# Optimization experiments

Measured on AMD Instinct MI355X. Metric: run time of the kernel, lower is better.

The kernel has to match this reference:

```python
import jax, jax.numpy as jnp
import numpy as np

# hardcoded constants from Model.sample_regions / gather_regions / __init__
RADIUS = 0.4
REGIONS = 50
BALL_K = 1000
TOP_K = 4
NEIGHBORHOOD = 128
COURSE = 512


def square_distance(src, dst):
    """src [B,N,C], dst [B,M,C] -> squared dists [B,N,M]."""
    d = -2.0 * jnp.einsum('bnc,bmc->bnm', src, dst)
    d = d + jnp.sum(src * src, -1)[:, :, None]
    d = d + jnp.sum(dst * dst, -1)[:, None, :]
    return d


def furthest_point_sample(xyz, npoint):
    """xyz [B,N,3] -> indices [B,npoint] (deterministic start at point 0)."""
    B, N, _ = xyz.shape
    barange = jnp.arange(B)

    def body(carry, _):
        dist, last = carry                      # dist [B,N], last [B] int32
        centroid = xyz[barange, last]           # [B,3]
        d = jnp.sum((xyz - centroid[:, None, :]) ** 2, -1)
        dist = jnp.minimum(dist, d)
        nxt = jnp.argmax(dist, axis=-1).astype(jnp.int32)
        return (dist, nxt), last

    init = (jnp.full((B, N), 1e10, xyz.dtype), jnp.zeros((B,), jnp.int32))
    _, idxs = jax.lax.scan(body, init, None, length=npoint)
    return jnp.transpose(idxs)                  # [B, npoint]


def knn_point(k, xyz, new_xyz):
    """k-NN of new_xyz [B,S,3] among xyz [B,N,3] -> idx [B,S,k]."""
    d = square_distance(new_xyz, xyz)
    _, idx = jax.lax.top_k(-d, k)
    return idx


def gather_xyz(xyz, idx):
    """xyz [B,N,3], idx [B,S] -> [B,S,3]."""
    B = xyz.shape[0]
    return xyz[jnp.arange(B)[:, None], idx]


def gather_regions(p_xyz, a_xyz, radius):
    """p_xyz [B,N,3] points, a_xyz [B,A,3] anchors -> [B, TOP_K*NEIGHBORHOOD, 3]."""
    B = p_xyz.shape[0]
    d2 = square_distance(a_xyz, p_xyz)                       # [B,A,N]
    counts = jnp.minimum(jnp.sum(d2 < radius * radius, axis=2), BALL_K)
    _, topk_idx = jax.lax.top_k(counts, TOP_K)               # densest anchors [B,TOP_K]
    sel = gather_xyz(a_xyz, topk_idx)                        # [B,TOP_K,3]
    nidx = knn_point(NEIGHBORHOOD, p_xyz, sel)               # [B,TOP_K,NB]
    neigh = p_xyz[jnp.arange(B)[:, None, None], nidx]        # [B,TOP_K,NB,3]
    return neigh.reshape(B, TOP_K * NEIGHBORHOOD, 3)


def sample_regions(p_xyz, regions, r):
    anchors_idx = furthest_point_sample(p_xyz, regions)
    anchors = gather_xyz(p_xyz, anchors_idx)
    return gather_regions(p_xyz, anchors, r)


def setup_inputs() -> dict:
    key = jax.random.key(0)
    points = jax.random.normal(key, (16, 3, 16384), dtype=jnp.float32)
    return {"points": points}


def reference(points):
    # points [B,3,N] -> p_xyz [B,N,3]
    p_xyz = jnp.transpose(points, (0, 2, 1))
    roi1 = sample_regions(p_xyz, REGIONS, RADIUS)            # [B,512,3]
    roi2 = sample_regions(p_xyz, REGIONS, RADIUS)            # [B,512,3] (a == b == 0.4)
    fps_idx = furthest_point_sample(p_xyz, COURSE)           # [B,512]
    fps_pts = gather_xyz(p_xyz, fps_idx)                     # [B,512,3]
    return jnp.concatenate([roi1, roi2, fps_pts], axis=1)    # [B,1536,3]
```

## Files before the change

kernel.cpp:

```cpp
#include <hip/hip_runtime.h>
#include <stdint.h>

#define NPTS 16384
#define BATCH 16
#define FPS_N 512
#define NANCH 50
#define TOPK 4
#define NBH 128
#define BALLK 1000

#define FT 512
#define PAIRS 16

#define OFF_X2 0
#define OFF_Y2 65536
#define OFF_FPSIDX 131072
#define OFF_CNT    (OFF_FPSIDX + 2048)
#define OFF_WRED   (OFF_CNT + 256)
#define OFF_T4     (OFF_WRED + 128)
#define OFF_KNN    (OFF_T4 + 16)
#define SMEM_TOTAL (OFF_KNN + 512)

#define CTRL_XOR1 0xB1
#define CTRL_XOR2 0x4E
#define CTRL_ROR4 0x124
#define CTRL_ROR8 0x128

#define DPP_MAX64(v, CTRL) do {                                                   \
  unsigned int _lo = (unsigned int)(v);                                           \
  unsigned int _hi = (unsigned int)((v) >> 32);                                   \
  unsigned int _slo = (unsigned int)__builtin_amdgcn_update_dpp((int)_lo, (int)_lo, CTRL, 0xf, 0xf, false); \
  unsigned int _shi = (unsigned int)__builtin_amdgcn_update_dpp((int)_hi, (int)_hi, CTRL, 0xf, 0xf, false); \
  unsigned long long _o = (((unsigned long long)_shi) << 32) | _slo;              \
  if (_o > (v)) (v) = _o;                                                         \
} while (0)

#define DPP_MIN64(v, CTRL) do {                                                   \
  unsigned int _lo = (unsigned int)(v);                                           \
  unsigned int _hi = (unsigned int)((v) >> 32);                                   \
  unsigned int _slo = (unsigned int)__builtin_amdgcn_update_dpp((int)_lo, (int)_lo, CTRL, 0xf, 0xf, false); \
  unsigned int _shi = (unsigned int)__builtin_amdgcn_update_dpp((int)_hi, (int)_hi, CTRL, 0xf, 0xf, false); \
  unsigned long long _o = (((unsigned long long)_shi) << 32) | _slo;              \
  if (_o < (v)) (v) = _o;                                                         \
} while (0)

#define SWZ16_MIN64(v) do {                                                       \
  unsigned int _lo = (unsigned int)(v), _hi = (unsigned int)((v) >> 32);          \
  unsigned int _slo = (unsigned int)__builtin_amdgcn_ds_swizzle((int)_lo, 0x401f);\
  unsigned int _shi = (unsigned int)__builtin_amdgcn_ds_swizzle((int)_hi, 0x401f);\
  unsigned long long _o = (((unsigned long long)_shi) << 32) | _slo;              \
  if (_o < (v)) (v) = _o;                                                         \
} while (0)

#define SHF32_MIN64(v) do {                                                       \
  unsigned long long _o = __shfl_xor((v), 32, 64);                                \
  if (_o < (v)) (v) = _o;                                                         \
} while (0)

__device__ __forceinline__ uint32_t f2key(float f) {
  uint32_t u = __float_as_uint(f);
  return (u & 0x80000000u) ? ~u : (u | 0x80000000u);
}

__global__ __launch_bounds__(FT, 2) void mega_kernel(const float* __restrict__ pts,
                                                     float* __restrict__ out) {
  extern __shared__ char smem[];
  float2* __restrict__ X2 = (float2*)(smem + OFF_X2);
  float2* __restrict__ Y2 = (float2*)(smem + OFF_Y2);
  int* __restrict__ fpsidx = (int*)(smem + OFF_FPSIDX);
  int* __restrict__ cnt = (int*)(smem + OFF_CNT);
  unsigned long long* __restrict__ wred = (unsigned long long*)(smem + OFF_WRED);
  int* __restrict__ t4 = (int*)(smem + OFF_T4);
  int* __restrict__ knnidx = (int*)(smem + OFF_KNN);

  const int bid = blockIdx.x;
  const bool isFps = bid < BATCH;
  const int b = isFps ? bid : ((bid - BATCH) >> 2);
  const int j = isFps ? 0 : ((bid - BATCH) & 3);
  const int nsteps = isFps ? FPS_N : NANCH;

  const int t = threadIdx.x;
  const int wS = __builtin_amdgcn_readfirstlane(t >> 6);
  const float* __restrict__ px = pts + (size_t)b * 3 * NPTS;
  const float* __restrict__ py = px + NPTS;
  const float* __restrict__ pz = py + NPTS;

  float2 z2[PAIRS], dist2[PAIRS];
#pragma unroll
  for (int k = 0; k < PAIRS; ++k) {
    const int i2 = (k << 10) + (t << 1);
    X2[(k << 9) + t] = *(const float2*)&px[i2];
    Y2[(k << 9) + t] = *(const float2*)&py[i2];
    z2[k] = *(const float2*)&pz[i2];
    dist2[k] = make_float2(1e10f, 1e10f);
  }
  if (t == 0) fpsidx[0] = 0;
  float bx = px[0], by = py[0], bz = pz[0];
  __syncthreads();

  for (int step = 1; step < nsteps; ++step) {
    const float nbx = -bx, nby = -by, nbz = -bz;
    const float2 nbx2 = make_float2(nbx, nbx);
    const float2 nby2 = make_float2(nby, nby);
    const float2 nbz2 = make_float2(nbz, nbz);
    float run = -1.0f;
#pragma unroll
    for (int k = 0; k < PAIRS; ++k) {
      const float2 Xp = X2[(k << 9) + t];
      const float2 Yp = Y2[(k << 9) + t];
      float2 t0, t1, t2;
      asm("v_pk_add_f32 %0, %3, %6\n\t"
          "v_pk_add_f32 %1, %4, %7\n\t"
          "v_pk_add_f32 %2, %5, %8\n\t"
          "v_pk_mul_f32 %0, %0, %0\n\t"
          "v_pk_mul_f32 %1, %1, %1\n\t"
          "v_pk_mul_f32 %2, %2, %2\n\t"
          "v_pk_add_f32 %0, %0, %1\n\t"
          "v_pk_add_f32 %0, %0, %2"
          : "=&v"(t0), "=&v"(t1), "=&v"(t2)
          : "v"(Xp), "v"(Yp), "v"(z2[k]), "v"(nbx2), "v"(nby2), "v"(nbz2));
      dist2[k].x = fminf(dist2[k].x, t0.x);
      dist2[k].y = fminf(dist2[k].y, t0.y);
      asm("v_max3_f32 %0, %0, %1, %2"
          : "+v"(run) : "v"(dist2[k].x), "v"(dist2[k].y));
    }
    uint32_t m = __float_as_uint(run);
    {
      uint32_t s;
      s = (uint32_t)__builtin_amdgcn_update_dpp((int)m, (int)m, CTRL_XOR1, 0xf, 0xf, false); m = m > s ? m : s;
      s = (uint32_t)__builtin_amdgcn_update_dpp((int)m, (int)m, CTRL_XOR2, 0xf, 0xf, false); m = m > s ? m : s;
      s = (uint32_t)__builtin_amdgcn_update_dpp((int)m, (int)m, CTRL_ROR4, 0xf, 0xf, false); m = m > s ? m : s;
      s = (uint32_t)__builtin_amdgcn_update_dpp((int)m, (int)m, CTRL_ROR8, 0xf, 0xf, false); m = m > s ? m : s;
      s = (uint32_t)__builtin_amdgcn_ds_swizzle((int)m, 0x401f);                              m = m > s ? m : s;
      s = (uint32_t)__shfl_xor((int)m, 32, 64);                                              m = m > s ? m : s;
    }
    const float gmaxf = __uint_as_float(m);
    uint32_t widx_w = 0xFFFFFFFFu;
#pragma unroll
    for (int k = 0; k < PAIRS; ++k) {
      const unsigned long long b0 = __ballot(dist2[k].x == gmaxf);
      const unsigned long long b1 = __ballot(dist2[k].y == gmaxf);
      const unsigned long long cb = b0 | b1;
      if (cb) {
        const int l = (int)__builtin_ctzll(cb);
        const uint32_t p = ((b0 >> l) & 1ull) ? 0u : 1u;
        const uint32_t cand = ((uint32_t)k << 10) + ((uint32_t)((wS << 6) | l) << 1) + p;
        widx_w = widx_w < cand ? widx_w : cand;
      }
    }
    const unsigned long long key =
        ((unsigned long long)m << 32) | (uint32_t)(~widx_w);
    const int par = step & 1;
    if ((t & 63) == 0) wred[par * 8 + wS] = key;
    __syncthreads();
    unsigned long long g = wred[par * 8 + (t & 7)];
    DPP_MAX64(g, CTRL_XOR1);
    DPP_MAX64(g, CTRL_XOR2);
    DPP_MAX64(g, CTRL_ROR4);
    const uint32_t widx = ~(uint32_t)g;
    if (t == 0) fpsidx[step] = (int)widx;
    const int si = __builtin_amdgcn_readfirstlane((int)widx);
    bx = px[si]; by = py[si]; bz = pz[si];
  }

  if (isFps) {
    __syncthreads();
    const int idx = fpsidx[t];
    const float X = px[idx], Y = py[idx], Z = pz[idx];
    float* o = out + ((size_t)b * 1536 + 1024 + t) * 3;
    o[0] = X; o[1] = Y; o[2] = Z;
    return;
  }

  const float R2 = (float)(0.4 * 0.4);

  if (t < 64) cnt[t] = 0;
  __syncthreads();
  for (int a = 0; a < NANCH; ++a) {
    const int ai = fpsidx[a];
    const float ax = px[ai], ay = py[ai], az = pz[ai];
    const float asum = __fadd_rn(__fadd_rn(__fmul_rn(ax, ax), __fmul_rn(ay, ay)),
                                 __fmul_rn(az, az));
    int local = 0;
#pragma unroll
    for (int k = 0; k < PAIRS; ++k) {
      const float2 Xp = X2[(k << 9) + t];
      const float2 Yp = Y2[(k << 9) + t];
      const float2 Zp = z2[k];
      {
        const float dot = __fadd_rn(__fadd_rn(__fmul_rn(ax, Xp.x), __fmul_rn(ay, Yp.x)),
                                    __fmul_rn(az, Zp.x));
        const float ps = __fadd_rn(__fadd_rn(__fmul_rn(Xp.x, Xp.x), __fmul_rn(Yp.x, Yp.x)),
                                   __fmul_rn(Zp.x, Zp.x));
        const float d = __fadd_rn(__fadd_rn(__fmul_rn(-2.0f, dot), asum), ps);
        local += (d < R2) ? 1 : 0;
      }
      {
        const float dot = __fadd_rn(__fadd_rn(__fmul_rn(ax, Xp.y), __fmul_rn(ay, Yp.y)),
                                    __fmul_rn(az, Zp.y));
        const float ps = __fadd_rn(__fadd_rn(__fmul_rn(Xp.y, Xp.y), __fmul_rn(Yp.y, Yp.y)),
                                   __fmul_rn(Zp.y, Zp.y));
        const float d = __fadd_rn(__fadd_rn(__fmul_rn(-2.0f, dot), asum), ps);
        local += (d < R2) ? 1 : 0;
      }
    }
#pragma unroll
    for (int off = 32; off > 0; off >>= 1) local += __shfl_xor(local, off, 64);
    if ((t & 63) == 0) atomicAdd(&cnt[a], local);
  }
  __syncthreads();

  if (t == 0) {
    unsigned long long used = 0ULL;
    for (int r = 0; r < TOPK; ++r) {
      int bestc = -1, besta = 0;
      for (int a = 0; a < NANCH; ++a) {
        if (used & (1ULL << a)) continue;
        int c = cnt[a];
        c = c < BALLK ? c : BALLK;
        if (c > bestc) { bestc = c; besta = a; }
      }
      used |= 1ULL << besta;
      t4[r] = fpsidx[besta];
    }
  }
  __syncthreads();

  const int ai = t4[j];
  const float ax = px[ai], ay = py[ai], az = pz[ai];
  const float asum = __fadd_rn(__fadd_rn(__fmul_rn(ax, ax), __fmul_rn(ay, ay)),
                               __fmul_rn(az, az));
  unsigned long long kk[2 * PAIRS];
#pragma unroll
  for (int k = 0; k < PAIRS; ++k) {
    const int i2 = (k << 10) + (t << 1);
    const float2 Xp = X2[(k << 9) + t];
    const float2 Yp = Y2[(k << 9) + t];
    const float2 Zp = z2[k];
    {
      const float dot = __fadd_rn(__fadd_rn(__fmul_rn(ax, Xp.x), __fmul_rn(ay, Yp.x)),
                                  __fmul_rn(az, Zp.x));
      const float ps = __fadd_rn(__fadd_rn(__fmul_rn(Xp.x, Xp.x), __fmul_rn(Yp.x, Yp.x)),
                                 __fmul_rn(Zp.x, Zp.x));
      const float d = __fadd_rn(__fadd_rn(__fmul_rn(-2.0f, dot), asum), ps);
      kk[2 * k] = ((unsigned long long)f2key(d) << 32) | (uint32_t)i2;
    }
    {
      const float dot = __fadd_rn(__fadd_rn(__fmul_rn(ax, Xp.y), __fmul_rn(ay, Yp.y)),
                                  __fmul_rn(az, Zp.y));
      const float ps = __fadd_rn(__fadd_rn(__fmul_rn(Xp.y, Xp.y), __fmul_rn(Yp.y, Yp.y)),
                                 __fmul_rn(Zp.y, Zp.y));
      const float d = __fadd_rn(__fadd_rn(__fmul_rn(-2.0f, dot), asum), ps);
      kk[2 * k + 1] = ((unsigned long long)f2key(d) << 32) | (uint32_t)(i2 + 1);
    }
  }
  for (int r = 0; r < NBH; ++r) {
    unsigned long long v16[16];
#pragma unroll
    for (int k = 0; k < 16; ++k) v16[k] = kk[2 * k] < kk[2 * k + 1] ? kk[2 * k] : kk[2 * k + 1];
#pragma unroll
    for (int k = 0; k < 8; ++k) v16[k] = v16[k] < v16[k + 8] ? v16[k] : v16[k + 8];
#pragma unroll
    for (int k = 0; k < 4; ++k) v16[k] = v16[k] < v16[k + 4] ? v16[k] : v16[k + 4];
    unsigned long long m0 = v16[0] < v16[2] ? v16[0] : v16[2];
    unsigned long long m1 = v16[1] < v16[3] ? v16[1] : v16[3];
    unsigned long long m = m0 < m1 ? m0 : m1;

    DPP_MIN64(m, CTRL_XOR1);
    DPP_MIN64(m, CTRL_XOR2);
    DPP_MIN64(m, CTRL_ROR4);
    DPP_MIN64(m, CTRL_ROR8);
    SWZ16_MIN64(m);
    SHF32_MIN64(m);

    const int par = r & 1;
    if ((t & 63) == 0) wred[par * 8 + wS] = m;
    __syncthreads();
    unsigned long long g = wred[par * 8 + (t & 7)];
    DPP_MIN64(g, CTRL_XOR1);
    DPP_MIN64(g, CTRL_XOR2);
    DPP_MIN64(g, CTRL_ROR4);
    if (t == 0) knnidx[r] = (int)(uint32_t)g;
#pragma unroll
    for (int k = 0; k < 2 * PAIRS; ++k)
      if (kk[k] == g) kk[k] = ~0ULL;
  }
  __syncthreads();

  if (t < NBH) {
    const int idx = knnidx[t];
    const float X = px[idx], Y = py[idx], Z = pz[idx];
    float* o1 = out + ((size_t)b * 1536 + (j << 7) + t) * 3;
    float* o2 = o1 + 512 * 3;
    o1[0] = X; o1[1] = Y; o1[2] = Z;
    o2[0] = X; o2[1] = Y; o2[2] = Z;
  }
}

extern "C" void kernel_launch(void* const* d_in, const int* in_sizes, int n_in,
                              void* d_out, int out_size, void* d_ws, size_t ws_size,
                              hipStream_t stream) {
  const float* pts = (const float*)d_in[0];
  float* out = (float*)d_out;
  (void)d_ws; (void)ws_size;

  hipFuncSetAttribute((const void*)mega_kernel,
                      hipFuncAttributeMaxDynamicSharedMemorySize, SMEM_TOTAL);
  mega_kernel<<<dim3(BATCH + BATCH * TOPK), dim3(FT), SMEM_TOTAL, stream>>>(pts, out);
}
```

Measured before the change: 987.2 us.

## Keep point coordinates in registers and broadcast FPS winner coords via LDS

Moves the X/Y coordinate arrays from LDS into per-thread registers, so the FPS loop no longer reads LDS on every step. Each wave's winning point coordinates are published to shared memory and broadcast with a shuffle, which removes the dependent global load of the selected point per step. The ball-count and kNN distance passes switch to packed f32 math with precomputed point norms, and counts use ballot plus popcount. The cost is much higher register pressure (x2, y2, z2, dist2 and ps2 per thread), and packed math may change rounding compared with the separately rounded scalar path.

```diff
diff --git a/kernel.cpp b/kernel.cpp
--- a/kernel.cpp
+++ b/kernel.cpp
@@ -11,15 +11,7 @@
 
 #define FT 512
 #define PAIRS 16
-
-#define OFF_X2 0
-#define OFF_Y2 65536
-#define OFF_FPSIDX 131072
-#define OFF_CNT    (OFF_FPSIDX + 2048)
-#define OFF_WRED   (OFF_CNT + 256)
-#define OFF_T4     (OFF_WRED + 128)
-#define OFF_KNN    (OFF_T4 + 16)
-#define SMEM_TOTAL (OFF_KNN + 512)
+#define NW 8
 
 #define CTRL_XOR1 0xB1
 #define CTRL_XOR2 0x4E
@@ -64,50 +56,58 @@
 
 __global__ __launch_bounds__(FT, 2) void mega_kernel(const float* __restrict__ pts,
                                                      float* __restrict__ out) {
-  extern __shared__ char smem[];
-  float2* __restrict__ X2 = (float2*)(smem + OFF_X2);
-  float2* __restrict__ Y2 = (float2*)(smem + OFF_Y2);
-  int* __restrict__ fpsidx = (int*)(smem + OFF_FPSIDX);
-  int* __restrict__ cnt = (int*)(smem + OFF_CNT);
-  unsigned long long* __restrict__ wred = (unsigned long long*)(smem + OFF_WRED);
-  int* __restrict__ t4 = (int*)(smem + OFF_T4);
-  int* __restrict__ knnidx = (int*)(smem + OFF_KNN);
+  __shared__ unsigned long long s_key[2][NW];
+  __shared__ float4 s_xyz[2][NW];
+  __shared__ float4 s_anch[NANCH];
+  __shared__ int s_cnt[NANCH];
+  __shared__ int s_t4[TOPK];
+  __shared__ int s_knn[NBH];
 
   const int bid = blockIdx.x;
   const bool isFps = bid < BATCH;
   const int b = isFps ? bid : ((bid - BATCH) >> 2);
-  const int j = isFps ? 0 : ((bid - BATCH) & 3);
+  const int j = (bid - BATCH) & 3;
   const int nsteps = isFps ? FPS_N : NANCH;
 
   const int t = threadIdx.x;
-  const int wS = __builtin_amdgcn_readfirstlane(t >> 6);
+  const int lane = t & 63;
+  const int wS = t >> 6;
   const float* __restrict__ px = pts + (size_t)b * 3 * NPTS;
   const float* __restrict__ py = px + NPTS;
   const float* __restrict__ pz = py + NPTS;
 
-  float2 z2[PAIRS], dist2[PAIRS];
+  float2 x2[PAIRS], y2[PAIRS], z2[PAIRS], dist2[PAIRS];
 #pragma unroll
   for (int k = 0; k < PAIRS; ++k) {
     const int i2 = (k << 10) + (t << 1);
-    X2[(k << 9) + t] = *(const float2*)&px[i2];
-    Y2[(k << 9) + t] = *(const float2*)&py[i2];
+    x2[k] = *(const float2*)&px[i2];
+    y2[k] = *(const float2*)&py[i2];
     z2[k] = *(const float2*)&pz[i2];
     dist2[k] = make_float2(1e10f, 1e10f);
   }
-  if (t == 0) fpsidx[0] = 0;
+#pragma unroll
+  for (int k = 0; k < PAIRS; ++k) {
+    asm volatile("" : "+v"(x2[k]), "+v"(y2[k]), "+v"(z2[k]));
+  }
+
   float bx = px[0], by = py[0], bz = pz[0];
-  __syncthreads();
+  if (t == 0) {
+    if (isFps) {
+      float* o = out + ((size_t)b * 1536 + 1024) * 3;
+      o[0] = bx; o[1] = by; o[2] = bz;
+    } else {
+      s_anch[0] = make_float4(bx, by, bz, 0.f);
+    }
+  }
 
   for (int step = 1; step < nsteps; ++step) {
-    const float nbx = -bx, nby = -by, nbz = -bz;
-    const float2 nbx2 = make_float2(nbx, nbx);
-    const float2 nby2 = make_float2(nby, nby);
-    const float2 nbz2 = make_float2(nbz, nbz);
+    const int par = step & 1;
+    const float2 nbx2 = make_float2(-bx, -bx);
+    const float2 nby2 = make_float2(-by, -by);
+    const float2 nbz2 = make_float2(-bz, -bz);
     float run = -1.0f;
 #pragma unroll
     for (int k = 0; k < PAIRS; ++k) {
-      const float2 Xp = X2[(k << 9) + t];
-      const float2 Yp = Y2[(k << 9) + t];
       float2 t0, t1, t2;
       asm("v_pk_add_f32 %0, %3, %6\n\t"
           "v_pk_add_f32 %1, %4, %7\n\t"
@@ -118,7 +118,7 @@
           "v_pk_add_f32 %0, %0, %1\n\t"
           "v_pk_add_f32 %0, %0, %2"
           : "=&v"(t0), "=&v"(t1), "=&v"(t2)
-          : "v"(Xp), "v"(Yp), "v"(z2[k]), "v"(nbx2), "v"(nby2), "v"(nbz2));
+          : "v"(x2[k]), "v"(y2[k]), "v"(z2[k]), "v"(nbx2), "v"(nby2), "v"(nbz2));
       dist2[k].x = fminf(dist2[k].x, t0.x);
       dist2[k].y = fminf(dist2[k].y, t0.y);
       asm("v_max3_f32 %0, %0, %1, %2"
@@ -135,78 +135,96 @@
       s = (uint32_t)__shfl_xor((int)m, 32, 64);                                              m = m > s ? m : s;
     }
     const float gmaxf = __uint_as_float(m);
-    uint32_t widx_w = 0xFFFFFFFFu;
+    uint32_t widx_w = 0u;
+    bool done = false;
 #pragma unroll
     for (int k = 0; k < PAIRS; ++k) {
       const unsigned long long b0 = __ballot(dist2[k].x == gmaxf);
       const unsigned long long b1 = __ballot(dist2[k].y == gmaxf);
       const unsigned long long cb = b0 | b1;
-      if (cb) {
+      if (!done && cb) {
         const int l = (int)__builtin_ctzll(cb);
         const uint32_t p = ((b0 >> l) & 1ull) ? 0u : 1u;
-        const uint32_t cand = ((uint32_t)k << 10) + ((uint32_t)((wS << 6) | l) << 1) + p;
-        widx_w = widx_w < cand ? widx_w : cand;
+        widx_w = ((uint32_t)k << 10) + ((uint32_t)((wS << 6) | l) << 1) + p;
+        if (lane == l) {
+          const float cx = p ? x2[k].y : x2[k].x;
+          const float cy = p ? y2[k].y : y2[k].x;
+          const float cz = p ? z2[k].y : z2[k].x;
+          s_xyz[par][wS] = make_float4(cx, cy, cz, 0.f);
+        }
+        done = true;
       }
     }
-    const unsigned long long key =
-        ((unsigned long long)m << 32) | (uint32_t)(~widx_w);
-    const int par = step & 1;
-    if ((t & 63) == 0) wred[par * 8 + wS] = key;
+    if (lane == 0)
+      s_key[par][wS] = ((unsigned long long)m << 32) | (uint32_t)(~widx_w);
     __syncthreads();
-    unsigned long long g = wred[par * 8 + (t & 7)];
+    unsigned long long g = s_key[par][lane & 7];
+    const float4 cand = s_xyz[par][lane & 7];
     DPP_MAX64(g, CTRL_XOR1);
     DPP_MAX64(g, CTRL_XOR2);
     DPP_MAX64(g, CTRL_ROR4);
     const uint32_t widx = ~(uint32_t)g;
-    if (t == 0) fpsidx[step] = (int)widx;
-    const int si = __builtin_amdgcn_readfirstlane((int)widx);
-    bx = px[si]; by = py[si]; bz = pz[si];
-  }
-
-  if (isFps) {
-    __syncthreads();
-    const int idx = fpsidx[t];
-    const float X = px[idx], Y = py[idx], Z = pz[idx];
-    float* o = out + ((size_t)b * 1536 + 1024 + t) * 3;
-    o[0] = X; o[1] = Y; o[2] = Z;
-    return;
-  }
+    const int wstar = (int)((widx >> 7) & 7);
+    bx = __shfl(cand.x, wstar, 64);
+    by = __shfl(cand.y, wstar, 64);
+    bz = __shfl(cand.z, wstar, 64);
+    if (t == 0) {
+      if (isFps) {
+        float* o = out + ((size_t)b * 1536 + 1024 + step) * 3;
+        o[0] = bx; o[1] = by; o[2] = bz;
+      } else {
+        s_anch[step] = make_float4(bx, by, bz, 0.f);
+      }
+    }
+  }
+  if (isFps) return;
+
+  float2 ps2[PAIRS];
+#pragma unroll
+  for (int k = 0; k < PAIRS; ++k) {
+    float2 s0, s1, s2;
+    asm("v_pk_mul_f32 %0, %3, %3\n\t"
+        "v_pk_mul_f32 %1, %4, %4\n\t"
+        "v_pk_mul_f32 %2, %5, %5\n\t"
+        "v_pk_add_f32 %0, %0, %1\n\t"
+        "v_pk_add_f32 %0, %0, %2"
+        : "=&v"(s0), "=&v"(s1), "=&v"(s2)
+        : "v"(x2[k]), "v"(y2[k]), "v"(z2[k]));
+    ps2[k] = s0;
+  }
+  if (t < NANCH) s_cnt[t] = 0;
+  __syncthreads();
 
   const float R2 = (float)(0.4 * 0.4);
-
-  if (t < 64) cnt[t] = 0;
-  __syncthreads();
+  const float2 mm2 = make_float2(-2.0f, -2.0f);
   for (int a = 0; a < NANCH; ++a) {
-    const int ai = fpsidx[a];
-    const float ax = px[ai], ay = py[ai], az = pz[ai];
+    const float4 A = s_anch[a];
+    const float ax = A.x, ay = A.y, az = A.z;
     const float asum = __fadd_rn(__fadd_rn(__fmul_rn(ax, ax), __fmul_rn(ay, ay)),
                                  __fmul_rn(az, az));
-    int local = 0;
+    const float2 ax2 = make_float2(ax, ax);
+    const float2 ay2 = make_float2(ay, ay);
+    const float2 az2 = make_float2(az, az);
+    const float2 as2 = make_float2(asum, asum);
+    int cw = 0;
 #pragma unroll
     for (int k = 0; k < PAIRS; ++k) {
-      const float2 Xp = X2[(k << 9) + t];
-      const float2 Yp = Y2[(k << 9) + t];
-      const float2 Zp = z2[k];
-      {
-        const float dot = __fadd_rn(__fadd_rn(__fmul_rn(ax, Xp.x), __fmul_rn(ay, Yp.x)),
-                                    __fmul_rn(az, Zp.x));
-        const float ps = __fadd_rn(__fadd_rn(__fmul_rn(Xp.x, Xp.x), __fmul_rn(Yp.x, Yp.x)),
-                                   __fmul_rn(Zp.x, Zp.x));
-        const float d = __fadd_rn(__fadd_rn(__fmul_rn(-2.0f, dot), asum), ps);
-        local += (d < R2) ? 1 : 0;
-      }
-      {
-        const float dot = __fadd_rn(__fadd_rn(__fmul_rn(ax, Xp.y), __fmul_rn(ay, Yp.y)),
-                                    __fmul_rn(az, Zp.y));
-        const float ps = __fadd_rn(__fadd_rn(__fmul_rn(Xp.y, Xp.y), __fmul_rn(Yp.y, Yp.y)),
-                                   __fmul_rn(Zp.y, Zp.y));
-        const float d = __fadd_rn(__fadd_rn(__fmul_rn(-2.0f, dot), asum), ps);
-        local += (d < R2) ? 1 : 0;
-      }
-    }
-#pragma unroll
-    for (int off = 32; off > 0; off >>= 1) local += __shfl_xor(local, off, 64);
-    if ((t & 63) == 0) atomicAdd(&cnt[a], local);
+      float2 d0, d1, d2v;
+      asm("v_pk_mul_f32 %0, %3, %6\n\t"
+          "v_pk_mul_f32 %1, %4, %7\n\t"
+          "v_pk_mul_f32 %2, %5, %8\n\t"
+          "v_pk_add_f32 %0, %0, %1\n\t"
+          "v_pk_add_f32 %0, %0, %2\n\t"
+          "v_pk_mul_f32 %0, %0, %9\n\t"
+          "v_pk_add_f32 %0, %0, %10\n\t"
+          "v_pk_add_f32 %0, %0, %11"
+          : "=&v"(d0), "=&v"(d1), "=&v"(d2v)
+          : "v"(x2[k]), "v"(y2[k]), "v"(z2[k]), "v"(ax2), "v"(ay2), "v"(az2),
+            "v"(mm2), "v"(as2), "v"(ps2[k]));
+      cw += (int)__popcll(__ballot(d0.x < R2));
+      cw += (int)__popcll(__ballot(d0.y < R2));
+    }
+    if (lane == 0) atomicAdd(&s_cnt[a], cw);
   }
   __syncthreads();
 
@@ -216,48 +234,48 @@
       int bestc = -1, besta = 0;
       for (int a = 0; a < NANCH; ++a) {
         if (used & (1ULL << a)) continue;
-        int c = cnt[a];
+        int c = s_cnt[a];
         c = c < BALLK ? c : BALLK;
         if (c > bestc) { bestc = c; besta = a; }
       }
       used |= 1ULL << besta;
-      t4[r] = fpsidx[besta];
+      s_t4[r] = besta;
     }
   }
   __syncthreads();
 
-  const int ai = t4[j];
-  const float ax = px[ai], ay = py[ai], az = pz[ai];
+  const float4 A = s_anch[s_t4[j]];
+  const float ax = A.x, ay = A.y, az = A.z;
   const float asum = __fadd_rn(__fadd_rn(__fmul_rn(ax, ax), __fmul_rn(ay, ay)),
                                __fmul_rn(az, az));
+  const float2 ax2 = make_float2(ax, ax);
+  const float2 ay2 = make_float2(ay, ay);
+  const float2 az2 = make_float2(az, az);
+  const float2 as2 = make_float2(asum, asum);
   unsigned long long kk[2 * PAIRS];
 #pragma unroll
   for (int k = 0; k < PAIRS; ++k) {
+    float2 d0, d1, d2v;
+    asm("v_pk_mul_f32 %0, %3, %6\n\t"
+        "v_pk_mul_f32 %1, %4, %7\n\t"
+        "v_pk_mul_f32 %2, %5, %8\n\t"
+        "v_pk_add_f32 %0, %0, %1\n\t"
+        "v_pk_add_f32 %0, %0, %2\n\t"
+        "v_pk_mul_f32 %0, %0, %9\n\t"
+        "v_pk_add_f32 %0, %0, %10\n\t"
+        "v_pk_add_f32 %0, %0, %11"
+        : "=&v"(d0), "=&v"(d1), "=&v"(d2v)
+        : "v"(x2[k]), "v"(y2[k]), "v"(z2[k]), "v"(ax2), "v"(ay2), "v"(az2),
+          "v"(mm2), "v"(as2), "v"(ps2[k]));
     const int i2 = (k << 10) + (t << 1);
-    const float2 Xp = X2[(k << 9) + t];
-    const float2 Yp = Y2[(k << 9) + t];
-    const float2 Zp = z2[k];
-    {
-      const float dot = __fadd_rn(__fadd_rn(__fmul_rn(ax, Xp.x), __fmul_rn(ay, Yp.x)),
-                                  __fmul_rn(az, Zp.x));
-      const float ps = __fadd_rn(__fadd_rn(__fmul_rn(Xp.x, Xp.x), __fmul_rn(Yp.x, Yp.x)),
-                                 __fmul_rn(Zp.x, Zp.x));
-      const float d = __fadd_rn(__fadd_rn(__fmul_rn(-2.0f, dot), asum), ps);
-      kk[2 * k] = ((unsigned long long)f2key(d) << 32) | (uint32_t)i2;
-    }
-    {
-      const float dot = __fadd_rn(__fadd_rn(__fmul_rn(ax, Xp.y), __fmul_rn(ay, Yp.y)),
-                                  __fmul_rn(az, Zp.y));
-      const float ps = __fadd_rn(__fadd_rn(__fmul_rn(Xp.y, Xp.y), __fmul_rn(Yp.y, Yp.y)),
-                                 __fmul_rn(Zp.y, Zp.y));
-      const float d = __fadd_rn(__fadd_rn(__fmul_rn(-2.0f, dot), asum), ps);
-      kk[2 * k + 1] = ((unsigned long long)f2key(d) << 32) | (uint32_t)(i2 + 1);
-    }
+    kk[2 * k]     = ((unsigned long long)f2key(d0.x) << 32) | (uint32_t)i2;
+    kk[2 * k + 1] = ((unsigned long long)f2key(d0.y) << 32) | (uint32_t)(i2 + 1);
   }
   for (int r = 0; r < NBH; ++r) {
     unsigned long long v16[16];
 #pragma unroll
-    for (int k = 0; k < 16; ++k) v16[k] = kk[2 * k] < kk[2 * k + 1] ? kk[2 * k] : kk[2 * k + 1];
+    for (int k = 0; k < 16; ++k)
+      v16[k] = kk[2 * k] < kk[2 * k + 1] ? kk[2 * k] : kk[2 * k + 1];
 #pragma unroll
     for (int k = 0; k < 8; ++k) v16[k] = v16[k] < v16[k + 8] ? v16[k] : v16[k + 8];
 #pragma unroll
@@ -274,13 +292,13 @@
     SHF32_MIN64(m);
 
     const int par = r & 1;
-    if ((t & 63) == 0) wred[par * 8 + wS] = m;
+    if (lane == 0) s_key[par][wS] = m;
     __syncthreads();
-    unsigned long long g = wred[par * 8 + (t & 7)];
+    unsigned long long g = s_key[par][lane & 7];
     DPP_MIN64(g, CTRL_XOR1);
     DPP_MIN64(g, CTRL_XOR2);
     DPP_MIN64(g, CTRL_ROR4);
-    if (t == 0) knnidx[r] = (int)(uint32_t)g;
+    if (t == 0) s_knn[r] = (int)(uint32_t)g;
 #pragma unroll
     for (int k = 0; k < 2 * PAIRS; ++k)
       if (kk[k] == g) kk[k] = ~0ULL;
@@ -288,7 +306,7 @@
   __syncthreads();
 
   if (t < NBH) {
-    const int idx = knnidx[t];
+    const int idx = s_knn[t];
     const float X = px[idx], Y = py[idx], Z = pz[idx];
     float* o1 = out + ((size_t)b * 1536 + (j << 7) + t) * 3;
     float* o2 = o1 + 512 * 3;
@@ -303,8 +321,5 @@
   const float* pts = (const float*)d_in[0];
   float* out = (float*)d_out;
   (void)d_ws; (void)ws_size;
-
-  hipFuncSetAttribute((const void*)mega_kernel,
-                      hipFuncAttributeMaxDynamicSharedMemorySize, SMEM_TOTAL);
-  mega_kernel<<<dim3(BATCH + BATCH * TOPK), dim3(FT), SMEM_TOTAL, stream>>>(pts, out);
+  mega_kernel<<<dim3(BATCH + BATCH * TOPK), dim3(FT), 0, stream>>>(pts, out);
 }
```

Measured after the change: 988.3 us. About the same (+0.1%).
